# Performance work log

Hardware: AMD Instinct MI355X
Metric: run time of the kernel (lower is better)

Reference implementation:

```python
import jax, jax.numpy as jnp
import numpy as np

NUM_NODES = 100000
D = 256            # node_hidden_dim
H = 256            # edge_hidden_dim
P = 524288         # num_pairs


def setup_inputs() -> dict:
    key = jax.random.key(0)
    k1, k2, k3, k4, k5, k6 = jax.random.split(key, 6)
    h_nodes = jax.random.normal(k1, (NUM_NODES, D), dtype=jnp.float32)
    dst = jax.random.randint(k2, (P,), 0, NUM_NODES, dtype=jnp.int64)
    src = jax.random.randint(k3, (P,), 0, NUM_NODES, dtype=jnp.int64)
    # Bias-free MLP weights, stored as [in, out] so forward is x @ W
    s1 = 1.0 / np.sqrt(2 * D)
    s2 = 1.0 / np.sqrt(H)
    W1 = jax.random.uniform(k4, (2 * D, H), jnp.float32, -s1, s1)
    W2 = jax.random.uniform(k5, (H, H), jnp.float32, -s2, s2)
    W3 = jax.random.uniform(k6, (H, 2), jnp.float32, -s2, s2)
    return {"h_nodes": h_nodes, "dst": dst, "src": src, "W1": W1, "W2": W2, "W3": W3}


def reference(h_nodes, dst, src, W1, W2, W3):
    # gather src/dst embeddings and concat -> [P, 2D]
    h_pair = jnp.concatenate([h_nodes[dst], h_nodes[src]], axis=-1)
    x = jax.nn.relu(h_pair @ W1)   # [P, H]
    x = jax.nn.relu(x @ W2)        # [P, H]
    return x @ W3                  # [P, 2] edge logits
```

## Files before the change

kernel.cpp:

```cpp
#include <hip/hip_runtime.h>
#include <stdint.h>

typedef __attribute__((ext_vector_type(8))) short short8;
typedef __attribute__((ext_vector_type(4))) short short4v;
typedef __attribute__((ext_vector_type(4))) float floatx4;

__device__ __forceinline__ unsigned short f2bf(float x) {
  unsigned int u = __float_as_uint(x);
  u += 0x7fffu + ((u >> 16) & 1u);
  return (unsigned short)(u >> 16);
}
__device__ __forceinline__ float bf2f(unsigned short b) {
  return __uint_as_float(((unsigned int)b) << 16);
}
__device__ __forceinline__ unsigned int pk2bf(float lo, float hi) {
  return (unsigned int)f2bf(lo) | ((unsigned int)f2bf(hi) << 16);
}
__device__ __forceinline__ int sw3(int r) { return (r & 7) ^ (((r >> 3) & 1) * 3); }

__device__ __forceinline__ void gld16(const unsigned short* g, unsigned short* l) {
  __builtin_amdgcn_global_load_lds(
      (const __attribute__((address_space(1))) void*)g,
      (__attribute__((address_space(3))) void*)l, 16, 0, 0);
}

__global__ void prep_kernel(const float* __restrict__ h, const float* __restrict__ W1,
                            const float* __restrict__ W2, const float* __restrict__ W3,
                            unsigned short* __restrict__ HBF, unsigned short* __restrict__ W1F,
                            unsigned short* __restrict__ W2F, unsigned short* __restrict__ W3F,
                            int nh8) {
  const int t = threadIdx.x;
  int b = blockIdx.x;
  if (b < 512) {
    int u = b * 256 + t;
    int j = u & 7, kq = (u >> 3) & 3, n = (u >> 5) & 255, k32 = u >> 13;
    W1F[u] = f2bf(W1[(k32 * 32 + kq * 8 + j) * 256 + n]);
    return;
  }
  b -= 512;
  if (b < 256) {
    int u = b * 256 + t;
    int j = u & 7, kq = (u >> 3) & 3, n = (u >> 5) & 255, k32 = u >> 13;
    W2F[u] = f2bf(W2[(k32 * 32 + kq * 8 + j) * 256 + n]);
    return;
  }
  b -= 256;
  if (b < 16) {
    int u = b * 256 + t;
    int j = u & 7, L = (u >> 3) & 63, k32 = u >> 9;
    int n = L & 15, kq = L >> 4;
    W3F[u] = (n < 2) ? f2bf(W3[(k32 * 32 + kq * 8 + j) * 2 + n]) : (unsigned short)0;
    return;
  }
  b -= 16;
  int u = b * 256 + t;
  if (u < nh8) {
    const float4* h4 = (const float4*)h;
    float4 v0 = h4[u * 2], v1 = h4[u * 2 + 1];
    short8 s;
    s[0] = (short)f2bf(v0.x); s[1] = (short)f2bf(v0.y);
    s[2] = (short)f2bf(v0.z); s[3] = (short)f2bf(v0.w);
    s[4] = (short)f2bf(v1.x); s[5] = (short)f2bf(v1.y);
    s[6] = (short)f2bf(v1.z); s[7] = (short)f2bf(v1.w);
    ((short8*)HBF)[u] = s;
  }
}

__global__ __launch_bounds__(256, 2)
void edge_mlp3(const unsigned short* __restrict__ hbf,
               const int* __restrict__ dst,
               const int* __restrict__ src,
               const unsigned short* __restrict__ W1F,
               const unsigned short* __restrict__ W2F,
               const unsigned short* __restrict__ W3F,
               float* __restrict__ out) {
  __shared__ __align__(16) unsigned short P[64 * 256];
  __shared__ __align__(16) unsigned short S[64 * 256];
  __shared__ int ioff[128];

  const int t = threadIdx.x, lane = t & 63, w = t >> 6;
  const int lq = lane >> 4, lm = lane & 15;
  const int m0 = blockIdx.x * 64;
  const int mm = lane & 31, rh = lane >> 5, rbase = w * 16;

  if (t < 64)       ioff[t] = dst[m0 + t];
  else if (t < 128) ioff[t] = src[m0 + t - 64];
  __syncthreads();

#pragma unroll
  for (int tt = 0; tt < 8; ++tt) {
    int rl = rbase + 2 * tt + rh;
    int node = ioff[rl];
    gld16(hbf + (size_t)node * 256 + ((mm ^ sw3(rl)) << 3), &P[(rbase + 2 * tt) * 256]);
  }
#pragma unroll
  for (int tt = 0; tt < 8; ++tt) {
    int rl = rbase + 2 * tt + rh;
    int node = ioff[64 + rl];
    gld16(hbf + (size_t)node * 256 + ((mm ^ sw3(rl)) << 3), &S[(rbase + 2 * tt) * 256]);
  }

  floatx4 acc[4][4];
#pragma unroll
  for (int i = 0; i < 4; ++i)
#pragma unroll
    for (int j = 0; j < 4; ++j) acc[i][j] = (floatx4)(0.0f);

  const short8* B1 = (const short8*)W1F;
  const short8* B2 = (const short8*)W2F;

  asm volatile("s_waitcnt vmcnt(8)" ::: "memory");
  __builtin_amdgcn_sched_barrier(0);
  __builtin_amdgcn_s_barrier();
  __builtin_amdgcn_sched_barrier(0);

  {
    short8 bq[2][4];
#pragma unroll
    for (int jt = 0; jt < 4; ++jt) bq[0][jt] = B1[(0 * 256 + w * 64 + jt * 16 + lm) * 4 + lq];
#pragma unroll
    for (int jt = 0; jt < 4; ++jt) bq[1][jt] = B1[(1 * 256 + w * 64 + jt * 16 + lm) * 4 + lq];

#pragma unroll
    for (int s = 0; s < 8; ++s) {
#pragma unroll
      for (int i = 0; i < 4; ++i) {
        int r = i * 16 + lm, c = s * 4 + lq;
        short8 af = *(const short8*)&P[r * 256 + ((c ^ sw3(r)) << 3)];
#pragma unroll
        for (int j = 0; j < 4; ++j)
          acc[i][j] = __builtin_amdgcn_mfma_f32_16x16x32_bf16(bq[s & 1][j], af, acc[i][j], 0, 0, 0);
      }
      if (s < 6)
#pragma unroll
        for (int jt = 0; jt < 4; ++jt)
          bq[s & 1][jt] = B1[((s + 2) * 256 + w * 64 + jt * 16 + lm) * 4 + lq];
    }
  }
  __syncthreads();

  {
    short8 bq[2][4];
#pragma unroll
    for (int jt = 0; jt < 4; ++jt) bq[0][jt] = B1[(8 * 256 + w * 64 + jt * 16 + lm) * 4 + lq];
#pragma unroll
    for (int jt = 0; jt < 4; ++jt) bq[1][jt] = B1[(9 * 256 + w * 64 + jt * 16 + lm) * 4 + lq];

#pragma unroll
    for (int s = 0; s < 8; ++s) {
#pragma unroll
      for (int i = 0; i < 4; ++i) {
        int r = i * 16 + lm, c = s * 4 + lq;
        short8 af = *(const short8*)&S[r * 256 + ((c ^ sw3(r)) << 3)];
#pragma unroll
        for (int j = 0; j < 4; ++j)
          acc[i][j] = __builtin_amdgcn_mfma_f32_16x16x32_bf16(bq[s & 1][j], af, acc[i][j], 0, 0, 0);
      }
      if (s < 6)
#pragma unroll
        for (int jt = 0; jt < 4; ++jt)
          bq[s & 1][jt] = B1[((s + 10) * 256 + w * 64 + jt * 16 + lm) * 4 + lq];
    }
  }

#pragma unroll
  for (int i = 0; i < 4; ++i) {
    int row = i * 16 + lm;
    int swz = sw3(row);
#pragma unroll
    for (int j = 0; j < 4; ++j) {
      int cb = w * 64 + j * 16 + lq * 4;
      int c8 = cb >> 3, ce = cb & 7;
      float v0 = fmaxf(acc[i][j][0], 0.0f);
      float v1 = fmaxf(acc[i][j][1], 0.0f);
      float v2 = fmaxf(acc[i][j][2], 0.0f);
      float v3 = fmaxf(acc[i][j][3], 0.0f);
      uint2 pv;
      pv.x = pk2bf(v0, v1);
      pv.y = pk2bf(v2, v3);
      *(uint2*)&P[row * 256 + (((c8 ^ swz) << 3) | ce)] = pv;
    }
  }
#pragma unroll
  for (int i = 0; i < 4; ++i)
#pragma unroll
    for (int j = 0; j < 4; ++j) acc[i][j] = (floatx4)(0.0f);
  __syncthreads();

  {
    short8 bq[2][4];
#pragma unroll
    for (int jt = 0; jt < 4; ++jt) bq[0][jt] = B2[(0 * 256 + w * 64 + jt * 16 + lm) * 4 + lq];
#pragma unroll
    for (int jt = 0; jt < 4; ++jt) bq[1][jt] = B2[(1 * 256 + w * 64 + jt * 16 + lm) * 4 + lq];

#pragma unroll
    for (int s = 0; s < 8; ++s) {
#pragma unroll
      for (int i = 0; i < 4; ++i) {
        int r = i * 16 + lm, c = s * 4 + lq;
        short8 af = *(const short8*)&P[r * 256 + ((c ^ sw3(r)) << 3)];
#pragma unroll
        for (int j = 0; j < 4; ++j)
          acc[i][j] = __builtin_amdgcn_mfma_f32_16x16x32_bf16(bq[s & 1][j], af, acc[i][j], 0, 0, 0);
      }
      if (s < 6)
#pragma unroll
        for (int jt = 0; jt < 4; ++jt)
          bq[s & 1][jt] = B2[((s + 2) * 256 + w * 64 + jt * 16 + lm) * 4 + lq];
    }
  }
  __syncthreads();

#pragma unroll
  for (int i = 0; i < 4; ++i) {
    int row = i * 16 + lm;
    int swz = sw3(row);
#pragma unroll
    for (int j = 0; j < 4; ++j) {
      int cb = w * 64 + j * 16 + lq * 4;
      int c8 = cb >> 3, ce = cb & 7;
      float v0 = fmaxf(acc[i][j][0], 0.0f);
      float v1 = fmaxf(acc[i][j][1], 0.0f);
      float v2 = fmaxf(acc[i][j][2], 0.0f);
      float v3 = fmaxf(acc[i][j][3], 0.0f);
      uint2 pv;
      pv.x = pk2bf(v0, v1);
      pv.y = pk2bf(v2, v3);
      *(uint2*)&P[row * 256 + (((c8 ^ swz) << 3) | ce)] = pv;
    }
  }
  __syncthreads();

  {
    floatx4 a3 = (floatx4)(0.0f);
    const short8* B3 = (const short8*)W3F;
#pragma unroll
    for (int s = 0; s < 8; ++s) {
      short8 b3 = B3[s * 64 + lane];
      int r = w * 16 + lm, cch = s * 4 + lq;
      short8 af = *(const short8*)&P[r * 256 + ((cch ^ sw3(r)) << 3)];
      a3 = __builtin_amdgcn_mfma_f32_16x16x32_bf16(af, b3, a3, 0, 0, 0);
    }
    if (lm < 2) {
#pragma unroll
      for (int rg = 0; rg < 4; ++rg)
        out[(m0 + w * 16 + lq * 4 + rg) * 2 + lm] = a3[rg];
    }
  }
}

__global__ void wfrag_kernel(const float* __restrict__ W,
                             unsigned short* __restrict__ out, int total) {
  int u = blockIdx.x * 256 + threadIdx.x;
  if (u >= total) return;
  int j = u & 7, kq = (u >> 3) & 3, n = (u >> 5) & 255, k32 = u >> 13;
  out[u] = f2bf(W[(k32 * 32 + kq * 8 + j) * 256 + n]);
}

__global__ __launch_bounds__(256, 2)
void edge_mlp_fb(const float* __restrict__ h,
                 const int* __restrict__ dst,
                 const int* __restrict__ src,
                 const unsigned short* __restrict__ W1F,
                 const unsigned short* __restrict__ W2F,
                 const float* __restrict__ W3,
                 float* __restrict__ out) {
  __shared__ unsigned short A[64 * 512];
  __shared__ float w3s[512];
  __shared__ int ioff[128];
  unsigned short* X = A;
  const int t = threadIdx.x, lane = t & 63, w = t >> 6;
  const int lq = lane >> 4, lm = lane & 15;
  const int m0 = blockIdx.x * 64;
  if (t < 64) ioff[t] = dst[m0 + t];
  else if (t < 128) ioff[t] = src[m0 + t - 64];
  w3s[t] = W3[t];
  w3s[t + 256] = W3[t + 256];
  __syncthreads();
  {
    const int c = lane, half = (c >= 32) ? 64 : 0, cc = c & 31;
#pragma unroll
    for (int it = 0; it < 16; ++it) {
      int r = it * 4 + w;
      int node = ioff[half + r];
      const float4* h4 = (const float4*)h;
      float4 v0 = h4[node * 64 + cc * 2], v1 = h4[node * 64 + cc * 2 + 1];
      short8 v;
      v[0] = (short)f2bf(v0.x); v[1] = (short)f2bf(v0.y);
      v[2] = (short)f2bf(v0.z); v[3] = (short)f2bf(v0.w);
      v[4] = (short)f2bf(v1.x); v[5] = (short)f2bf(v1.y);
      v[6] = (short)f2bf(v1.z); v[7] = (short)f2bf(v1.w);
      *(short8*)&A[r * 512 + ((c ^ (r & 7)) << 3)] = v;
    }
  }
  floatx4 acc[4][4];
#pragma unroll
  for (int i = 0; i < 4; ++i)
#pragma unroll
    for (int j = 0; j < 4; ++j) acc[i][j] = (floatx4)(0.0f);
  __syncthreads();
  const short8* B1 = (const short8*)W1F;
  const short8* B2 = (const short8*)W2F;
#pragma unroll
  for (int k32 = 0; k32 < 16; ++k32) {
    short8 b[4], af[4];
#pragma unroll
    for (int jt = 0; jt < 4; ++jt)
      b[jt] = B1[(k32 * 256 + w * 64 + jt * 16 + lm) * 4 + lq];
#pragma unroll
    for (int i = 0; i < 4; ++i) {
      int r = i * 16 + lm, c = k32 * 4 + lq;
      af[i] = *(const short8*)&A[r * 512 + ((c ^ (r & 7)) << 3)];
    }
#pragma unroll
    for (int i = 0; i < 4; ++i)
#pragma unroll
      for (int j = 0; j < 4; ++j)
        acc[i][j] = __builtin_amdgcn_mfma_f32_16x16x32_bf16(af[i], b[j], acc[i][j], 0, 0, 0);
  }
  __syncthreads();
#pragma unroll
  for (int i = 0; i < 4; ++i) {
    int row0 = i * 16 + lq * 4;
#pragma unroll
    for (int j = 0; j < 4; ++j) {
      int col = w * 64 + j * 16 + lm, c8 = col >> 3, ce = col & 7;
#pragma unroll
      for (int rg = 0; rg < 4; ++rg) {
        int row = row0 + rg;
        float v = acc[i][j][rg];
        v = v > 0.0f ? v : 0.0f;
        X[row * 256 + (((c8 ^ (row & 7)) << 3) | ce)] = f2bf(v);
      }
    }
  }
#pragma unroll
  for (int i = 0; i < 4; ++i)
#pragma unroll
    for (int j = 0; j < 4; ++j) acc[i][j] = (floatx4)(0.0f);
  __syncthreads();
#pragma unroll
  for (int k32 = 0; k32 < 8; ++k32) {
    short8 b[4], af[4];
#pragma unroll
    for (int jt = 0; jt < 4; ++jt)
      b[jt] = B2[(k32 * 256 + w * 64 + jt * 16 + lm) * 4 + lq];
#pragma unroll
    for (int i = 0; i < 4; ++i) {
      int r = i * 16 + lm, c = k32 * 4 + lq;
      af[i] = *(const short8*)&X[r * 256 + ((c ^ (r & 7)) << 3)];
    }
#pragma unroll
    for (int i = 0; i < 4; ++i)
#pragma unroll
      for (int j = 0; j < 4; ++j)
        acc[i][j] = __builtin_amdgcn_mfma_f32_16x16x32_bf16(af[i], b[j], acc[i][j], 0, 0, 0);
  }
  __syncthreads();
#pragma unroll
  for (int i = 0; i < 4; ++i) {
    int row0 = i * 16 + lq * 4;
#pragma unroll
    for (int j = 0; j < 4; ++j) {
      int col = w * 64 + j * 16 + lm, c8 = col >> 3, ce = col & 7;
#pragma unroll
      for (int rg = 0; rg < 4; ++rg) {
        int row = row0 + rg;
        float v = acc[i][j][rg];
        v = v > 0.0f ? v : 0.0f;
        X[row * 256 + (((c8 ^ (row & 7)) << 3) | ce)] = f2bf(v);
      }
    }
  }
  __syncthreads();
  {
    int r = t >> 2, o = (t >> 1) & 1, hh = t & 1;
    float s = 0.0f;
#pragma unroll
    for (int it = 0; it < 16; ++it) {
      int c = hh * 16 + it;
      short8 xv = *(const short8*)&X[r * 256 + ((c ^ (r & 7)) << 3)];
#pragma unroll
      for (int e = 0; e < 8; ++e)
        s += bf2f((unsigned short)xv[e]) * w3s[((c << 3) + e) * 2 + o];
    }
    s += __shfl_xor(s, 1);
    if (hh == 0) out[(m0 + r) * 2 + o] = s;
  }
}

extern "C" void kernel_launch(void* const* d_in, const int* in_sizes, int n_in,
                              void* d_out, int out_size, void* d_ws, size_t ws_size,
                              hipStream_t stream) {
  const float* h   = (const float*)d_in[0];
  const int*   dst = (const int*)d_in[1];
  const int*   src = (const int*)d_in[2];
  const float* W1  = (const float*)d_in[3];
  const float* W2  = (const float*)d_in[4];
  const float* W3  = (const float*)d_in[5];
  float* out = (float*)d_out;

  const int h_elems = in_sizes[0];
  const int n_pairs = in_sizes[1];
  const int ntiles  = n_pairs / 64;

  const size_t hbf_elems = (size_t)h_elems;
  const bool use_hbf =
      ws_size >= (hbf_elems + 131072 + 65536 + 4096) * sizeof(unsigned short);

  unsigned short* HBF = (unsigned short*)d_ws;
  unsigned short* W1F = HBF + hbf_elems;
  unsigned short* W2F = W1F + 131072;
  unsigned short* W3F = W2F + 65536;

  if (use_hbf) {
    int nh8 = h_elems / 8;
    int grid = 512 + 256 + 16 + (nh8 + 255) / 256;
    prep_kernel<<<grid, 256, 0, stream>>>(h, W1, W2, W3, HBF, W1F, W2F, W3F, nh8);
    edge_mlp3<<<ntiles, 256, 0, stream>>>(HBF, dst, src, W1F, W2F, W3F, out);
  } else {
    unsigned short* W1Fb = (unsigned short*)d_ws;
    unsigned short* W2Fb = W1Fb + 131072;
    wfrag_kernel<<<512, 256, 0, stream>>>(W1, W1Fb, 131072);
    wfrag_kernel<<<256, 256, 0, stream>>>(W2, W2Fb, 65536);
    edge_mlp_fb<<<ntiles, 256, 0, stream>>>(h, dst, src, W1Fb, W2Fb, W3, out);
  }
}
```

Measured before the change: 401.1 us.

## Halve LDS by staging src rows in registers and reusing one buffer

Replaces the two 32KB shared tiles with a single tile. The src embedding gather is loaded into registers during the dst-half GEMM, then written into the shared tile once the first half finishes. This cuts LDS per block so more blocks can be resident to hide gather latency. In exchange it adds extra barriers, extra VGPR pressure from the 8 staged vectors, and a separate LDS write pass.

New measurement: 438.6 us. 9.4% more time.

```diff
diff --git a/kernel.cpp b/kernel.cpp
--- a/kernel.cpp
+++ b/kernel.cpp
@@ -74,8 +74,7 @@
                const unsigned short* __restrict__ W2F,
                const unsigned short* __restrict__ W3F,
                float* __restrict__ out) {
-  __shared__ __align__(16) unsigned short P[64 * 256];
-  __shared__ __align__(16) unsigned short S[64 * 256];
+  __shared__ __align__(16) unsigned short A[64 * 256];
   __shared__ int ioff[128];
 
   const int t = threadIdx.x, lane = t & 63, w = t >> 6;
@@ -91,13 +90,14 @@
   for (int tt = 0; tt < 8; ++tt) {
     int rl = rbase + 2 * tt + rh;
     int node = ioff[rl];
-    gld16(hbf + (size_t)node * 256 + ((mm ^ sw3(rl)) << 3), &P[(rbase + 2 * tt) * 256]);
-  }
+    gld16(hbf + (size_t)node * 256 + ((mm ^ sw3(rl)) << 3), &A[(rbase + 2 * tt) * 256]);
+  }
+  short8 g[8];
 #pragma unroll
   for (int tt = 0; tt < 8; ++tt) {
     int rl = rbase + 2 * tt + rh;
     int node = ioff[64 + rl];
-    gld16(hbf + (size_t)node * 256 + ((mm ^ sw3(rl)) << 3), &S[(rbase + 2 * tt) * 256]);
+    g[tt] = *(const short8*)(hbf + (size_t)node * 256 + ((mm ^ sw3(rl)) << 3));
   }
 
   floatx4 acc[4][4];
@@ -109,10 +109,7 @@
   const short8* B1 = (const short8*)W1F;
   const short8* B2 = (const short8*)W2F;
 
-  asm volatile("s_waitcnt vmcnt(8)" ::: "memory");
-  __builtin_amdgcn_sched_barrier(0);
-  __builtin_amdgcn_s_barrier();
-  __builtin_amdgcn_sched_barrier(0);
+  __syncthreads();
 
   {
     short8 bq[2][4];
@@ -126,7 +123,7 @@
 #pragma unroll
       for (int i = 0; i < 4; ++i) {
         int r = i * 16 + lm, c = s * 4 + lq;
-        short8 af = *(const short8*)&P[r * 256 + ((c ^ sw3(r)) << 3)];
+        short8 af = *(const short8*)&A[r * 256 + ((c ^ sw3(r)) << 3)];
 #pragma unroll
         for (int j = 0; j < 4; ++j)
           acc[i][j] = __builtin_amdgcn_mfma_f32_16x16x32_bf16(bq[s & 1][j], af, acc[i][j], 0, 0, 0);
@@ -139,6 +136,11 @@
   }
   __syncthreads();
 
+#pragma unroll
+  for (int tt = 0; tt < 8; ++tt)
+    *(short8*)&A[(rbase + 2 * tt) * 256 + lane * 8] = g[tt];
+  __syncthreads();
+
   {
     short8 bq[2][4];
 #pragma unroll
@@ -151,7 +153,7 @@
 #pragma unroll
       for (int i = 0; i < 4; ++i) {
         int r = i * 16 + lm, c = s * 4 + lq;
-        short8 af = *(const short8*)&S[r * 256 + ((c ^ sw3(r)) << 3)];
+        short8 af = *(const short8*)&A[r * 256 + ((c ^ sw3(r)) << 3)];
 #pragma unroll
         for (int j = 0; j < 4; ++j)
           acc[i][j] = __builtin_amdgcn_mfma_f32_16x16x32_bf16(bq[s & 1][j], af, acc[i][j], 0, 0, 0);
@@ -162,6 +164,7 @@
           bq[s & 1][jt] = B1[((s + 10) * 256 + w * 64 + jt * 16 + lm) * 4 + lq];
     }
   }
+  __syncthreads();
 
 #pragma unroll
   for (int i = 0; i < 4; ++i) {
@@ -178,7 +181,7 @@
       uint2 pv;
       pv.x = pk2bf(v0, v1);
       pv.y = pk2bf(v2, v3);
-      *(uint2*)&P[row * 256 + (((c8 ^ swz) << 3) | ce)] = pv;
+      *(uint2*)&A[row * 256 + (((c8 ^ swz) << 3) | ce)] = pv;
     }
   }
 #pragma unroll
@@ -199,7 +202,7 @@
 #pragma unroll
       for (int i = 0; i < 4; ++i) {
         int r = i * 16 + lm, c = s * 4 + lq;
-        short8 af = *(const short8*)&P[r * 256 + ((c ^ sw3(r)) << 3)];
+        short8 af = *(const short8*)&A[r * 256 + ((c ^ sw3(r)) << 3)];
 #pragma unroll
         for (int j = 0; j < 4; ++j)
           acc[i][j] = __builtin_amdgcn_mfma_f32_16x16x32_bf16(bq[s & 1][j], af, acc[i][j], 0, 0, 0);
@@ -227,7 +230,7 @@
       uint2 pv;
       pv.x = pk2bf(v0, v1);
       pv.y = pk2bf(v2, v3);
-      *(uint2*)&P[row * 256 + (((c8 ^ swz) << 3) | ce)] = pv;
+      *(uint2*)&A[row * 256 + (((c8 ^ swz) << 3) | ce)] = pv;
     }
   }
   __syncthreads();
@@ -239,7 +242,7 @@
     for (int s = 0; s < 8; ++s) {
       short8 b3 = B3[s * 64 + lane];
       int r = w * 16 + lm, cch = s * 4 + lq;
-      short8 af = *(const short8*)&P[r * 256 + ((cch ^ sw3(r)) << 3)];
+      short8 af = *(const short8*)&A[r * 256 + ((cch ^ sw3(r)) << 3)];
       a3 = __builtin_amdgcn_mfma_f32_16x16x32_bf16(af, b3, a3, 0, 0, 0);
     }
     if (lm < 2) {
```

## Split edge MLP work across eight waves per block with 2x4 wave tiling

Applied to the files above, without the earlier changes.

Doubles the block size to 512 threads and splits each block's 64x256 output tile so every wave computes 32 rows by 64 columns instead of 64 rows. Each wave gathers fewer node rows, and the early partial wait on the gather is replaced by a full barrier. The aim is more waves in flight to hide gather and LDS latency. The costs are twice the weight fragment loads per block, the loss of the gather/compute overlap, and a tighter register budget from the new launch bounds that may cause spills.

After: 553.7 us. 38.1% more time.

```diff
diff --git a/kernel.cpp b/kernel.cpp
--- a/kernel.cpp
+++ b/kernel.cpp
@@ -66,7 +66,7 @@
   }
 }
 
-__global__ __launch_bounds__(256, 2)
+__global__ __launch_bounds__(512, 4)
 void edge_mlp3(const unsigned short* __restrict__ hbf,
                const int* __restrict__ dst,
                const int* __restrict__ src,
@@ -80,52 +80,51 @@
 
   const int t = threadIdx.x, lane = t & 63, w = t >> 6;
   const int lq = lane >> 4, lm = lane & 15;
+  const int wr = (w & 1) * 32;
+  const int wc = (w >> 1) * 64;
   const int m0 = blockIdx.x * 64;
-  const int mm = lane & 31, rh = lane >> 5, rbase = w * 16;
+  const int mm = lane & 31, rh = lane >> 5, rbase = w * 8;
 
   if (t < 64)       ioff[t] = dst[m0 + t];
   else if (t < 128) ioff[t] = src[m0 + t - 64];
   __syncthreads();
 
 #pragma unroll
-  for (int tt = 0; tt < 8; ++tt) {
+  for (int tt = 0; tt < 4; ++tt) {
     int rl = rbase + 2 * tt + rh;
     int node = ioff[rl];
     gld16(hbf + (size_t)node * 256 + ((mm ^ sw3(rl)) << 3), &P[(rbase + 2 * tt) * 256]);
   }
 #pragma unroll
-  for (int tt = 0; tt < 8; ++tt) {
+  for (int tt = 0; tt < 4; ++tt) {
     int rl = rbase + 2 * tt + rh;
     int node = ioff[64 + rl];
     gld16(hbf + (size_t)node * 256 + ((mm ^ sw3(rl)) << 3), &S[(rbase + 2 * tt) * 256]);
   }
 
-  floatx4 acc[4][4];
-#pragma unroll
-  for (int i = 0; i < 4; ++i)
+  floatx4 acc[2][4];
+#pragma unroll
+  for (int i = 0; i < 2; ++i)
 #pragma unroll
     for (int j = 0; j < 4; ++j) acc[i][j] = (floatx4)(0.0f);
 
   const short8* B1 = (const short8*)W1F;
   const short8* B2 = (const short8*)W2F;
 
-  asm volatile("s_waitcnt vmcnt(8)" ::: "memory");
-  __builtin_amdgcn_sched_barrier(0);
-  __builtin_amdgcn_s_barrier();
-  __builtin_amdgcn_sched_barrier(0);
+  __syncthreads();
 
   {
     short8 bq[2][4];
 #pragma unroll
-    for (int jt = 0; jt < 4; ++jt) bq[0][jt] = B1[(0 * 256 + w * 64 + jt * 16 + lm) * 4 + lq];
-#pragma unroll
-    for (int jt = 0; jt < 4; ++jt) bq[1][jt] = B1[(1 * 256 + w * 64 + jt * 16 + lm) * 4 + lq];
+    for (int jt = 0; jt < 4; ++jt) bq[0][jt] = B1[(0 * 256 + wc + jt * 16 + lm) * 4 + lq];
+#pragma unroll
+    for (int jt = 0; jt < 4; ++jt) bq[1][jt] = B1[(1 * 256 + wc + jt * 16 + lm) * 4 + lq];
 
 #pragma unroll
     for (int s = 0; s < 8; ++s) {
 #pragma unroll
-      for (int i = 0; i < 4; ++i) {
-        int r = i * 16 + lm, c = s * 4 + lq;
+      for (int i = 0; i < 2; ++i) {
+        int r = wr + i * 16 + lm, c = s * 4 + lq;
         short8 af = *(const short8*)&P[r * 256 + ((c ^ sw3(r)) << 3)];
 #pragma unroll
         for (int j = 0; j < 4; ++j)
@@ -134,7 +133,7 @@
       if (s < 6)
 #pragma unroll
         for (int jt = 0; jt < 4; ++jt)
-          bq[s & 1][jt] = B1[((s + 2) * 256 + w * 64 + jt * 16 + lm) * 4 + lq];
+          bq[s & 1][jt] = B1[((s + 2) * 256 + wc + jt * 16 + lm) * 4 + lq];
     }
   }
   __syncthreads();
@@ -142,15 +141,15 @@
   {
     short8 bq[2][4];
 #pragma unroll
-    for (int jt = 0; jt < 4; ++jt) bq[0][jt] = B1[(8 * 256 + w * 64 + jt * 16 + lm) * 4 + lq];
-#pragma unroll
-    for (int jt = 0; jt < 4; ++jt) bq[1][jt] = B1[(9 * 256 + w * 64 + jt * 16 + lm) * 4 + lq];
+    for (int jt = 0; jt < 4; ++jt) bq[0][jt] = B1[(8 * 256 + wc + jt * 16 + lm) * 4 + lq];
+#pragma unroll
+    for (int jt = 0; jt < 4; ++jt) bq[1][jt] = B1[(9 * 256 + wc + jt * 16 + lm) * 4 + lq];
 
 #pragma unroll
     for (int s = 0; s < 8; ++s) {
 #pragma unroll
-      for (int i = 0; i < 4; ++i) {
-        int r = i * 16 + lm, c = s * 4 + lq;
+      for (int i = 0; i < 2; ++i) {
+        int r = wr + i * 16 + lm, c = s * 4 + lq;
         short8 af = *(const short8*)&S[r * 256 + ((c ^ sw3(r)) << 3)];
 #pragma unroll
         for (int j = 0; j < 4; ++j)
@@ -159,17 +158,17 @@
       if (s < 6)
 #pragma unroll
         for (int jt = 0; jt < 4; ++jt)
-          bq[s & 1][jt] = B1[((s + 10) * 256 + w * 64 + jt * 16 + lm) * 4 + lq];
-    }
-  }
-
-#pragma unroll
-  for (int i = 0; i < 4; ++i) {
-    int row = i * 16 + lm;
+          bq[s & 1][jt] = B1[((s + 10) * 256 + wc + jt * 16 + lm) * 4 + lq];
+    }
+  }
+
+#pragma unroll
+  for (int i = 0; i < 2; ++i) {
+    int row = wr + i * 16 + lm;
     int swz = sw3(row);
 #pragma unroll
     for (int j = 0; j < 4; ++j) {
-      int cb = w * 64 + j * 16 + lq * 4;
+      int cb = wc + j * 16 + lq * 4;
       int c8 = cb >> 3, ce = cb & 7;
       float v0 = fmaxf(acc[i][j][0], 0.0f);
       float v1 = fmaxf(acc[i][j][1], 0.0f);
@@ -182,7 +181,7 @@
     }
   }
 #pragma unroll
-  for (int i = 0; i < 4; ++i)
+  for (int i = 0; i < 2; ++i)
 #pragma unroll
     for (int j = 0; j < 4; ++j) acc[i][j] = (floatx4)(0.0f);
   __syncthreads();
@@ -190,15 +189,15 @@
   {
     short8 bq[2][4];
 #pragma unroll
-    for (int jt = 0; jt < 4; ++jt) bq[0][jt] = B2[(0 * 256 + w * 64 + jt * 16 + lm) * 4 + lq];
-#pragma unroll
-    for (int jt = 0; jt < 4; ++jt) bq[1][jt] = B2[(1 * 256 + w * 64 + jt * 16 + lm) * 4 + lq];
+    for (int jt = 0; jt < 4; ++jt) bq[0][jt] = B2[(0 * 256 + wc + jt * 16 + lm) * 4 + lq];
+#pragma unroll
+    for (int jt = 0; jt < 4; ++jt) bq[1][jt] = B2[(1 * 256 + wc + jt * 16 + lm) * 4 + lq];
 
 #pragma unroll
     for (int s = 0; s < 8; ++s) {
 #pragma unroll
-      for (int i = 0; i < 4; ++i) {
-        int r = i * 16 + lm, c = s * 4 + lq;
+      for (int i = 0; i < 2; ++i) {
+        int r = wr + i * 16 + lm, c = s * 4 + lq;
         short8 af = *(const short8*)&P[r * 256 + ((c ^ sw3(r)) << 3)];
 #pragma unroll
         for (int j = 0; j < 4; ++j)
@@ -207,18 +206,18 @@
       if (s < 6)
 #pragma unroll
         for (int jt = 0; jt < 4; ++jt)
-          bq[s & 1][jt] = B2[((s + 2) * 256 + w * 64 + jt * 16 + lm) * 4 + lq];
-    }
-  }
-  __syncthreads();
-
-#pragma unroll
-  for (int i = 0; i < 4; ++i) {
-    int row = i * 16 + lm;
+          bq[s & 1][jt] = B2[((s + 2) * 256 + wc + jt * 16 + lm) * 4 + lq];
+    }
+  }
+  __syncthreads();
+
+#pragma unroll
+  for (int i = 0; i < 2; ++i) {
+    int row = wr + i * 16 + lm;
     int swz = sw3(row);
 #pragma unroll
     for (int j = 0; j < 4; ++j) {
-      int cb = w * 64 + j * 16 + lq * 4;
+      int cb = wc + j * 16 + lq * 4;
       int c8 = cb >> 3, ce = cb & 7;
       float v0 = fmaxf(acc[i][j][0], 0.0f);
       float v1 = fmaxf(acc[i][j][1], 0.0f);
@@ -232,7 +231,7 @@
   }
   __syncthreads();
 
-  {
+  if (w < 4) {
     floatx4 a3 = (floatx4)(0.0f);
     const short8* B3 = (const short8*)W3F;
 #pragma unroll
@@ -418,7 +417,7 @@
     int nh8 = h_elems / 8;
     int grid = 512 + 256 + 16 + (nh8 + 255) / 256;
     prep_kernel<<<grid, 256, 0, stream>>>(h, W1, W2, W3, HBF, W1F, W2F, W3F, nh8);
-    edge_mlp3<<<ntiles, 256, 0, stream>>>(HBF, dst, src, W1F, W2F, W3F, out);
+    edge_mlp3<<<ntiles, 512, 0, stream>>>(HBF, dst, src, W1F, W2F, W3F, out);
   } else {
     unsigned short* W1Fb = (unsigned short*)d_ws;
     unsigned short* W2Fb = W1Fb + 131072;
```
